# Kernel optimization log

Measured on AMD Instinct MI355X. Metric: run time of the kernel, lower is better.

Reference implementation:

```python
import jax, jax.numpy as jnp
import numpy as np

B, T, C = 8, 2048, 1024
NEG_BIG = -1e30  # exp(NEG_BIG - row_max) underflows to exactly 0 in fp32


def setup_inputs() -> dict:
    key = jax.random.key(0)
    k1, k2 = jax.random.split(key)
    x = jax.random.normal(k1, (B, T, C), dtype=jnp.float32)
    # nn.Linear weight, shape [out, in]; forward computes x @ W^T
    W_H = jax.random.normal(k2, (C, C), dtype=jnp.float32) * (1.0 / np.sqrt(C))
    return {"x": x, "W_H": W_H}


def reference(x, W_H):
    Tdim = x.shape[1]
    xH = jnp.einsum('btc,dc->btd', x, W_H)          # H(x) = x @ W^T, [B,T,C]
    scores = jnp.einsum('btc,bsc->bts', x, xH)       # bilinear scores, [B,T,T]
    # tril_plus_one=True -> strictly-lower-triangular mask (diagonal=-1)
    mask = jnp.tril(jnp.ones((Tdim, Tdim), dtype=bool), k=-1)
    scores = jnp.where(mask, scores, NEG_BIG)
    wei = jax.nn.softmax(scores, axis=-1)            # fully-masked rows -> uniform, zeroed below
    all_masked = ~mask.any(axis=-1)                  # [T], True for row 0
    wei = jnp.where(all_masked[None, :, None], 0.0, wei)
    out = jnp.einsum('bts,bsc->btc', wei, xH)
    return -out
```

## Files before the change

### kernel.cpp

```cpp
#include <hip/hip_runtime.h>
#include <stdint.h>

#define Bn 8
#define Tn 2048
#define Cn 1024
#define Mn (Bn * Tn)
#define NTRI 136
#define NLIN2 72

typedef __attribute__((ext_vector_type(4))) float f32x4;
typedef _Float16 f16;
typedef __attribute__((ext_vector_type(8))) _Float16 f16x8;
typedef uint16_t u16;
typedef uint32_t u32;

static __device__ __forceinline__ u16 f2h(float f) {
  union { f16 h; u16 u; } c; c.h = (f16)f; return c.u;
}
static __device__ __forceinline__ f32x4 mfmaH(f16x8 a, f16x8 b, f32x4 c) {
  return __builtin_amdgcn_mfma_f32_16x16x32_f16(a, b, c, 0, 0, 0);
}
static __device__ __forceinline__ void gld16(const void* g, void* l) {
  __builtin_amdgcn_global_load_lds(
      (const __attribute__((address_space(1))) u32*)g,
      (__attribute__((address_space(3))) u32*)l, 16, 0, 0);
}

__global__ __launch_bounds__(256) void ksplitW(const float* __restrict__ s,
                                               u16* __restrict__ hi) {
  size_t i = ((size_t)blockIdx.x * 256 + threadIdx.x) * 8;
  float4 a = *(const float4*)(s + i), b = *(const float4*)(s + i + 4);
  float f[8] = {a.x, a.y, a.z, a.w, b.x, b.y, b.z, b.w};
  union { u16 u[8]; uint4 v; } H;
#pragma unroll
  for (int j = 0; j < 8; ++j) H.u[j] = f2h(f[j]);
  *(uint4*)(hi + i) = H.v;
}

__global__ __launch_bounds__(256) void ksplitX(const float* __restrict__ s,
                                               u16* __restrict__ hi,
                                               u16* __restrict__ lo) {
  size_t i = ((size_t)blockIdx.x * 256 + threadIdx.x) * 8;
  float4 a = *(const float4*)(s + i), b = *(const float4*)(s + i + 4);
  float f[8] = {a.x, a.y, a.z, a.w, b.x, b.y, b.z, b.w};
  union { u16 u[8]; uint4 v; } H, L;
#pragma unroll
  for (int j = 0; j < 8; ++j) {
    f16 h = (f16)f[j];
    union { f16 h; u16 u; } ch; ch.h = h;
    H.u[j] = ch.u;
    L.u[j] = f2h(f[j] - (float)h);
  }
  *(uint4*)(hi + i) = H.v;
  *(uint4*)(lo + i) = L.v;
}

__global__ __launch_bounds__(256) void k1_xh(const u16* __restrict__ x_h,
                                             const u16* __restrict__ W_h,
                                             u16* __restrict__ xh) {
  __shared__ __align__(16) u16 Ah[8192], Bh[8192];
  const int tid = threadIdx.x;
  const int m0 = blockIdx.x * 128, n0 = blockIdx.y * 128;
  const int wave = tid >> 6, lane = tid & 63;
  const int wrow = (wave >> 1) * 64, wcol = (wave & 1) * 64;
  const int quad = lane >> 4, l16 = lane & 15;

  f32x4 acc[4][4] = {};

  for (int k0 = 0; k0 < Cn; k0 += 64) {
#pragma unroll
    for (int i = 0; i < 4; ++i) {
      int chunk = i * 256 + tid;
      int kk = chunk >> 9, row = (chunk >> 2) & 127, c8 = (chunk & 3) * 8;
      gld16(x_h + (size_t)(m0 + row) * Cn + k0 + kk * 32 + c8, Ah + chunk * 8);
      gld16(W_h + (size_t)(n0 + row) * Cn + k0 + kk * 32 + c8, Bh + chunk * 8);
    }
    __syncthreads();
#pragma unroll
    for (int kk = 0; kk < 2; ++kk) {
      f16x8 a[4], b[4];
#pragma unroll
      for (int i = 0; i < 4; ++i) {
        a[i] = *(const f16x8*)(Ah + kk * 4096 + (wrow + i * 16 + l16) * 32 + quad * 8);
        b[i] = *(const f16x8*)(Bh + kk * 4096 + (wcol + i * 16 + l16) * 32 + quad * 8);
      }
#pragma unroll
      for (int mi = 0; mi < 4; ++mi)
#pragma unroll
        for (int ni = 0; ni < 4; ++ni)
          acc[mi][ni] = mfmaH(a[mi], b[ni], acc[mi][ni]);
    }
    __syncthreads();
  }
#pragma unroll
  for (int mi = 0; mi < 4; ++mi)
#pragma unroll
    for (int ni = 0; ni < 4; ++ni)
#pragma unroll
      for (int r = 0; r < 4; ++r) {
        int row = wrow + mi * 16 + quad * 4 + r;
        int col = wcol + ni * 16 + l16;
        xh[(size_t)(m0 + row) * Cn + n0 + col] = f2h(acc[mi][ni][r]);
      }
}

__global__ __launch_bounds__(512) void k2_scores(const u16* __restrict__ x_h,
                                                 const u16* __restrict__ x_l,
                                                 const u16* __restrict__ xh,
                                                 u16* __restrict__ P,
                                                 float* __restrict__ mt,
                                                 float* __restrict__ lt) {
  __shared__ __align__(16) union {
    struct { u16 Ah[3][4096], Al[3][4096], Bh[3][8192]; } s;
    struct { float Mrow[4][128]; float Lrow[4][128]; } e;
  } u;
  const int tid = threadIdx.x;
  const int bL = blockIdx.y;
  const int lin = blockIdx.x;
  int qt = 0, cum = 0;
  while (cum + ((qt >> 1) + 1) <= lin) { cum += (qt >> 1) + 1; qt++; }
  const int bcol = lin - cum;
  const int t0 = qt * 128, s0 = bcol * 256;
  const int wave = tid >> 6, lane = tid & 63;
  const int wc = wave & 3;
  const int wrow = (wave >> 2) * 64, wcol = wc * 64;
  const int quad = lane >> 4, l16 = lane & 15;

  f32x4 acc[4][4] = {};
  const size_t abase = ((size_t)bL * Tn + t0) * Cn;
  const size_t bbase = ((size_t)bL * Tn + s0) * Cn;
  const int arow = tid >> 2, ac8 = (tid & 3) * 8;

  auto stage = [&](int buf, int k0) {
    size_t aoff = abase + (size_t)arow * Cn + k0 + ac8;
    gld16(x_h + aoff, &u.s.Ah[buf][tid * 8]);
    gld16(x_l + aoff, &u.s.Al[buf][tid * 8]);
#pragma unroll
    for (int i = 0; i < 2; ++i) {
      int ch = i * 512 + tid;
      int row = ch >> 2, c8 = (ch & 3) * 8;
      gld16(xh + bbase + (size_t)row * Cn + k0 + c8, &u.s.Bh[buf][ch * 8]);
    }
  };

  stage(0, 0);
  stage(1, 32);
  int cur = 0;
#pragma unroll 1
  for (int kidx = 0; kidx < 32; ++kidx) {
    if (kidx < 31) {
      asm volatile("s_waitcnt vmcnt(4) lgkmcnt(0)" ::: "memory");
    } else {
      asm volatile("s_waitcnt vmcnt(0) lgkmcnt(0)" ::: "memory");
    }
    __builtin_amdgcn_s_barrier();
    __builtin_amdgcn_sched_barrier(0);
    if (kidx < 30) {
      int tgt = cur >= 1 ? cur - 1 : 2;
      stage(tgt, (kidx + 2) * 32);
    }
    f16x8 b[4];
#pragma unroll
    for (int ni = 0; ni < 4; ++ni)
      b[ni] = *(const f16x8*)&u.s.Bh[cur][(wcol + ni * 16 + l16) * 32 + quad * 8];
#pragma unroll
    for (int mi = 0; mi < 4; ++mi) {
      f16x8 ah = *(const f16x8*)&u.s.Ah[cur][(wrow + mi * 16 + l16) * 32 + quad * 8];
      f16x8 al = *(const f16x8*)&u.s.Al[cur][(wrow + mi * 16 + l16) * 32 + quad * 8];
#pragma unroll
      for (int ni = 0; ni < 4; ++ni) {
        acc[mi][ni] = mfmaH(ah, b[ni], acc[mi][ni]);
        acc[mi][ni] = mfmaH(al, b[ni], acc[mi][ni]);
      }
    }
    cur = cur < 2 ? cur + 1 : 0;
  }

  float rm[4][4];
#pragma unroll
  for (int mi = 0; mi < 4; ++mi)
#pragma unroll
    for (int r = 0; r < 4; ++r) {
      int row = wrow + mi * 16 + quad * 4 + r;
      float m = -1e30f;
#pragma unroll
      for (int ni = 0; ni < 4; ++ni) {
        int scol = s0 + wcol + ni * 16 + l16;
        if (scol >= t0 + row) acc[mi][ni][r] = -1e30f;
        m = fmaxf(m, acc[mi][ni][r]);
      }
      m = fmaxf(m, __shfl_xor(m, 1));
      m = fmaxf(m, __shfl_xor(m, 2));
      m = fmaxf(m, __shfl_xor(m, 4));
      m = fmaxf(m, __shfl_xor(m, 8));
      rm[mi][r] = m;
    }
  if (l16 == 0) {
#pragma unroll
    for (int mi = 0; mi < 4; ++mi)
#pragma unroll
      for (int r = 0; r < 4; ++r)
        u.e.Mrow[wc][wrow + mi * 16 + quad * 4 + r] = rm[mi][r];
  }
  __syncthreads();
  const int h2 = (wc >> 1) * 2;
  float rs[4][4];
#pragma unroll
  for (int mi = 0; mi < 4; ++mi)
#pragma unroll
    for (int r = 0; r < 4; ++r) {
      int row = wrow + mi * 16 + quad * 4 + r;
      float m2 = fmaxf(u.e.Mrow[h2][row], u.e.Mrow[h2 + 1][row]);
      float s = 0.f;
#pragma unroll
      for (int ni = 0; ni < 4; ++ni) {
        int scol = s0 + wcol + ni * 16 + l16;
        float p = (scol < t0 + row) ? __expf(acc[mi][ni][r] - m2) : 0.0f;
        acc[mi][ni][r] = p;
        s += p;
      }
      s += __shfl_xor(s, 1);
      s += __shfl_xor(s, 2);
      s += __shfl_xor(s, 4);
      s += __shfl_xor(s, 8);
      rs[mi][r] = s;
      rm[mi][r] = m2;
    }
  if (l16 == 0) {
#pragma unroll
    for (int mi = 0; mi < 4; ++mi)
#pragma unroll
      for (int r = 0; r < 4; ++r)
        u.e.Lrow[wc][wrow + mi * 16 + quad * 4 + r] = rs[mi][r];
  }
  __syncthreads();
  const int st128 = bcol * 2 + (wc >> 1);
  if (st128 <= qt) {
    if ((wc & 1) == 0 && l16 == 0) {
#pragma unroll
      for (int mi = 0; mi < 4; ++mi)
#pragma unroll
        for (int r = 0; r < 4; ++r) {
          int row = wrow + mi * 16 + quad * 4 + r;
          size_t rI = (size_t)bL * Tn + t0 + row;
          mt[rI * 16 + st128] = rm[mi][r];
          lt[rI * 16 + st128] = u.e.Lrow[wc][row] + u.e.Lrow[wc + 1][row];
        }
    }
    const size_t pbase = (size_t)(bL * NTRI + qt * (qt + 1) / 2 + st128) * 16384;
#pragma unroll
    for (int mi = 0; mi < 4; ++mi)
#pragma unroll
      for (int ni = 0; ni < 4; ++ni)
#pragma unroll
        for (int r = 0; r < 4; ++r) {
          int row = wrow + mi * 16 + quad * 4 + r;
          int pcol = (wcol & 64) + ni * 16 + l16;
          P[pbase + row * 128 + pcol] = f2h(acc[mi][ni][r]);
        }
  }
}

__global__ __launch_bounds__(256) void k3_stats(const float* __restrict__ mt,
                                                const float* __restrict__ lt,
                                                float* __restrict__ Mr,
                                                float* __restrict__ Li) {
  int r = blockIdx.x * 256 + threadIdx.x;
  int t = r & (Tn - 1);
  int nt = (t == 0) ? 0 : (((t - 1) >> 7) + 1);
  float M = -1e30f;
  for (int i = 0; i < nt; ++i) M = fmaxf(M, mt[(size_t)r * 16 + i]);
  float L = 0.f;
  for (int i = 0; i < nt; ++i) L += lt[(size_t)r * 16 + i] * __expf(mt[(size_t)r * 16 + i] - M);
  Mr[r] = M;
  Li[r] = (L > 0.f) ? 1.f / L : 0.f;
}

__global__ __launch_bounds__(256) void ktr(const u16* __restrict__ src,
                                           u16* __restrict__ dst) {
  __shared__ __align__(16) u16 S[128 * 136];
  const int t0 = blockIdx.x * 128, c0 = blockIdx.y * 128, b = blockIdx.z;
  const int tid = threadIdx.x;
#pragma unroll
  for (int i = 0; i < 8; ++i) {
    int chunk = tid + i * 256;
    int row = chunk >> 4, c8 = (chunk & 15) * 8;
    uint4 v = *(const uint4*)(src + ((size_t)b * Tn + t0 + row) * Cn + c0 + c8);
    *(uint4*)(S + row * 136 + c8) = v;
  }
  __syncthreads();
#pragma unroll
  for (int i = 0; i < 8; ++i) {
    int chunk = tid + i * 256;
    int crow = chunk >> 4, t8 = (chunk & 15) * 8;
    union { u16 s[8]; uint4 v; } o;
#pragma unroll
    for (int j = 0; j < 8; ++j) o.s[j] = S[(t8 + j) * 136 + crow];
    *(uint4*)(dst + ((size_t)b * Cn + c0 + crow) * Tn + t0 + t8) = o.v;
  }
}

__global__ __launch_bounds__(256) void k4_out(const u16* __restrict__ P,
                                              const u16* __restrict__ xhT,
                                              const float* __restrict__ mt,
                                              const float* __restrict__ Mr,
                                              const float* __restrict__ Li,
                                              float* __restrict__ out) {
  __shared__ __align__(16) u16 Ap[8192], Bp[8192];
  const int tid = threadIdx.x;
  const int tt = 15 - blockIdx.x;
  const int cn = blockIdx.y, bL = blockIdx.z;
  const int t0 = tt * 128, c0 = cn * 128;
  const int wave = tid >> 6, lane = tid & 63;
  const int wrow = (wave >> 1) * 64, wcol = (wave & 1) * 64;
  const int quad = lane >> 4, l16 = lane & 15;

  f32x4 acc[4][4] = {};
  size_t rI[4]; float MrL[4], LiL[4];
#pragma unroll
  for (int mi = 0; mi < 4; ++mi) {
    rI[mi] = (size_t)bL * Tn + t0 + wrow + mi * 16 + l16;
    MrL[mi] = Mr[rI[mi]];
    LiL[mi] = Li[rI[mi]];
  }
  const size_t bbase = ((size_t)bL * Cn + c0) * Tn;

  for (int st = 0; st <= tt; ++st) {
    f16 ah[4];
#pragma unroll
    for (int mi = 0; mi < 4; ++mi)
      ah[mi] = (f16)(__expf(mt[rI[mi] * 16 + st] - MrL[mi]) * LiL[mi]);
    const size_t pbase = (size_t)(bL * NTRI + tt * (tt + 1) / 2 + st) * 16384;
#pragma unroll 1
    for (int kl = 0; kl < 128; kl += 64) {
#pragma unroll
      for (int i = 0; i < 4; ++i) {
        int chunk = i * 256 + tid;
        int kk = chunk >> 9, row = (chunk >> 2) & 127, c8 = (chunk & 3) * 8;
        gld16(P + pbase + (size_t)row * 128 + kl + kk * 32 + c8, Ap + chunk * 8);
        gld16(xhT + bbase + (size_t)row * Tn + st * 128 + kl + kk * 32 + c8, Bp + chunk * 8);
      }
      __syncthreads();
#pragma unroll
      for (int kk = 0; kk < 2; ++kk) {
        f16x8 a[4], b[4];
#pragma unroll
        for (int i = 0; i < 4; ++i) {
          a[i] = *(const f16x8*)(Ap + kk * 4096 + (wrow + i * 16 + l16) * 32 + quad * 8);
          f16x8 sv;
#pragma unroll
          for (int j = 0; j < 8; ++j) sv[j] = ah[i];
          a[i] = a[i] * sv;
          b[i] = *(const f16x8*)(Bp + kk * 4096 + (wcol + i * 16 + l16) * 32 + quad * 8);
        }
#pragma unroll
        for (int mi = 0; mi < 4; ++mi)
#pragma unroll
          for (int ni = 0; ni < 4; ++ni)
            acc[mi][ni] = mfmaH(a[mi], b[ni], acc[mi][ni]);
      }
      __syncthreads();
    }
  }
#pragma unroll
  for (int mi = 0; mi < 4; ++mi)
#pragma unroll
    for (int ni = 0; ni < 4; ++ni)
#pragma unroll
      for (int r = 0; r < 4; ++r) {
        int row = wrow + mi * 16 + quad * 4 + r;
        int col = wcol + ni * 16 + l16;
        out[((size_t)bL * Tn + t0 + row) * Cn + c0 + col] = -acc[mi][ni][r];
      }
}

extern "C" void kernel_launch(void* const* d_in, const int* in_sizes, int n_in,
                              void* d_out, int out_size, void* d_ws, size_t ws_size,
                              hipStream_t stream) {
  (void)in_sizes; (void)n_in; (void)out_size;
  const float* x = (const float*)d_in[0];
  const float* W = (const float*)d_in[1];
  float* out = (float*)d_out;

  const size_t FULL_NEED = 3ull * Mn * Cn * 2 + (size_t)Bn * NTRI * 16384 * 2 +
                           (size_t)Cn * Cn * 2 + 2ull * Mn * 16 * 4 + 2ull * Mn * 4;
  const int nch = (ws_size >= FULL_NEED) ? 1 : 2;
  const int nb = Bn / nch;
  const size_t rowsC = (size_t)nb * Tn;
  const size_t sA = rowsC * Cn * 2;

  char* p = (char*)d_ws;
  u16* x_h = (u16*)p; p += sA;
  u16* xLT = (u16*)p; p += sA;
  u16* xh  = (u16*)p; p += sA;
  u16* Pp  = (u16*)p; p += (size_t)nb * NTRI * 16384 * 2;
  u16* W_h = (u16*)p; p += (size_t)Cn * Cn * 2;
  float* mt = (float*)p; p += rowsC * 16 * 4;
  float* lt = (float*)p; p += rowsC * 16 * 4;
  float* Mr = (float*)p; p += rowsC * 4;
  float* Li = (float*)p; p += rowsC * 4;

  dim3 blk(256);
  ksplitW<<<dim3(Cn * Cn / 2048), blk, 0, stream>>>(W, W_h);
  for (int c = 0; c < nch; ++c) {
    const float* xc = x + (size_t)c * rowsC * Cn;
    float* oc = out + (size_t)c * rowsC * Cn;
    ksplitX<<<dim3((u32)(rowsC * Cn / 2048)), blk, 0, stream>>>(xc, x_h, xLT);
    k1_xh<<<dim3((u32)(rowsC / 128), Cn / 128), blk, 0, stream>>>(x_h, W_h, xh);
    k2_scores<<<dim3(NLIN2, nb), dim3(512), 0, stream>>>(x_h, xLT, xh, Pp, mt, lt);
    k3_stats<<<dim3((u32)(rowsC / 256)), blk, 0, stream>>>(mt, lt, Mr, Li);
    ktr<<<dim3(Tn / 128, Cn / 128, nb), blk, 0, stream>>>(xh, xLT);
    k4_out<<<dim3(16, Cn / 128, nb), blk, 0, stream>>>(Pp, xLT, mt, Mr, Li, oc);
  }
}
```

Baseline: 413.3 us.

## Widen k4_out tile to 128x256 with triple-buffered LDS pipeline and precomputed alphas

The output GEMM kernel now uses 512 threads and 128x256 output tiles, halving the number of column blocks so each P tile is reused across more columns. The K loop is restructured into 32-wide steps with a three-stage LDS ring buffer, issuing loads two steps ahead with explicit vmcnt waits and one barrier per step instead of two. The per-row softmax scaling factors are precomputed once into LDS instead of recomputing exp per row and tile in registers. Risks are lower occupancy from larger blocks and LDS use, and fewer blocks for load balance across the triangular workload.

```diff
diff --git a/kernel.cpp b/kernel.cpp
--- a/kernel.cpp
+++ b/kernel.cpp
@@ -300,68 +300,94 @@
   }
 }
 
-__global__ __launch_bounds__(256) void k4_out(const u16* __restrict__ P,
+__global__ __launch_bounds__(512) void k4_out(const u16* __restrict__ P,
                                               const u16* __restrict__ xhT,
                                               const float* __restrict__ mt,
                                               const float* __restrict__ Mr,
                                               const float* __restrict__ Li,
                                               float* __restrict__ out) {
-  __shared__ __align__(16) u16 Ap[8192], Bp[8192];
+  __shared__ __align__(16) u16 Ap[3][4096], Bp[3][8192];
+  __shared__ u16 alphaLds[16 * 128];
   const int tid = threadIdx.x;
   const int tt = 15 - blockIdx.x;
   const int cn = blockIdx.y, bL = blockIdx.z;
-  const int t0 = tt * 128, c0 = cn * 128;
+  const int t0 = tt * 128, c0 = cn * 256;
   const int wave = tid >> 6, lane = tid & 63;
-  const int wrow = (wave >> 1) * 64, wcol = (wave & 1) * 64;
+  const int wc = wave & 3;
+  const int wrow = (wave >> 2) * 64, wcol = wc * 64;
   const int quad = lane >> 4, l16 = lane & 15;
 
+  {
+    const size_t rbase = (size_t)bL * Tn + t0;
+#pragma unroll
+    for (int j = 0; j < 4; ++j) {
+      int idx = tid + j * 512;
+      int stp = idx >> 7, row = idx & 127;
+      float a = 0.f;
+      if (stp <= tt)
+        a = __expf(mt[(rbase + row) * 16 + stp] - Mr[rbase + row]) * Li[rbase + row];
+      alphaLds[idx] = f2h(a);
+    }
+  }
+
   f32x4 acc[4][4] = {};
-  size_t rI[4]; float MrL[4], LiL[4];
-#pragma unroll
-  for (int mi = 0; mi < 4; ++mi) {
-    rI[mi] = (size_t)bL * Tn + t0 + wrow + mi * 16 + l16;
-    MrL[mi] = Mr[rI[mi]];
-    LiL[mi] = Li[rI[mi]];
-  }
   const size_t bbase = ((size_t)bL * Cn + c0) * Tn;
-
-  for (int st = 0; st <= tt; ++st) {
-    f16 ah[4];
-#pragma unroll
-    for (int mi = 0; mi < 4; ++mi)
-      ah[mi] = (f16)(__expf(mt[rI[mi] * 16 + st] - MrL[mi]) * LiL[mi]);
-    const size_t pbase = (size_t)(bL * NTRI + tt * (tt + 1) / 2 + st) * 16384;
+  const size_t ptile0 = (size_t)(bL * NTRI + tt * (tt + 1) / 2) * 16384;
+
+  auto stage = [&](int buf, int step) {
+    const int st = step >> 2, k32 = (step & 3) * 32;
+    {
+      int row = tid >> 2, c8 = (tid & 3) * 8;
+      gld16(P + ptile0 + (size_t)st * 16384 + row * 128 + k32 + c8,
+            &Ap[buf][tid * 8]);
+    }
+#pragma unroll
+    for (int i = 0; i < 2; ++i) {
+      int ch = i * 512 + tid;
+      int row = ch >> 2, c8 = (ch & 3) * 8;
+      gld16(xhT + bbase + (size_t)row * Tn + st * 128 + k32 + c8,
+            &Bp[buf][ch * 8]);
+    }
+  };
+
+  const int steps = 4 * (tt + 1);
+  stage(0, 0);
+  stage(1, 1);
+  int cur = 0;
 #pragma unroll 1
-    for (int kl = 0; kl < 128; kl += 64) {
-#pragma unroll
-      for (int i = 0; i < 4; ++i) {
-        int chunk = i * 256 + tid;
-        int kk = chunk >> 9, row = (chunk >> 2) & 127, c8 = (chunk & 3) * 8;
-        gld16(P + pbase + (size_t)row * 128 + kl + kk * 32 + c8, Ap + chunk * 8);
-        gld16(xhT + bbase + (size_t)row * Tn + st * 128 + kl + kk * 32 + c8, Bp + chunk * 8);
-      }
-      __syncthreads();
-#pragma unroll
-      for (int kk = 0; kk < 2; ++kk) {
-        f16x8 a[4], b[4];
-#pragma unroll
-        for (int i = 0; i < 4; ++i) {
-          a[i] = *(const f16x8*)(Ap + kk * 4096 + (wrow + i * 16 + l16) * 32 + quad * 8);
-          f16x8 sv;
-#pragma unroll
-          for (int j = 0; j < 8; ++j) sv[j] = ah[i];
-          a[i] = a[i] * sv;
-          b[i] = *(const f16x8*)(Bp + kk * 4096 + (wcol + i * 16 + l16) * 32 + quad * 8);
-        }
-#pragma unroll
-        for (int mi = 0; mi < 4; ++mi)
-#pragma unroll
-          for (int ni = 0; ni < 4; ++ni)
-            acc[mi][ni] = mfmaH(a[mi], b[ni], acc[mi][ni]);
-      }
-      __syncthreads();
-    }
-  }
+  for (int s = 0; s < steps; ++s) {
+    if (s < steps - 1) {
+      asm volatile("s_waitcnt vmcnt(3) lgkmcnt(0)" ::: "memory");
+    } else {
+      asm volatile("s_waitcnt vmcnt(0) lgkmcnt(0)" ::: "memory");
+    }
+    __builtin_amdgcn_s_barrier();
+    __builtin_amdgcn_sched_barrier(0);
+    if (s < steps - 2) {
+      int tgt = cur >= 1 ? cur - 1 : 2;
+      stage(tgt, s + 2);
+    }
+    const int st = s >> 2;
+    f16x8 b[4];
+#pragma unroll
+    for (int ni = 0; ni < 4; ++ni)
+      b[ni] = *(const f16x8*)&Bp[cur][(wcol + ni * 16 + l16) * 32 + quad * 8];
+#pragma unroll
+    for (int mi = 0; mi < 4; ++mi) {
+      union { u16 u; f16 h; } ca;
+      ca.u = alphaLds[st * 128 + wrow + mi * 16 + l16];
+      f16x8 sv;
+#pragma unroll
+      for (int j = 0; j < 8; ++j) sv[j] = ca.h;
+      f16x8 a = *(const f16x8*)&Ap[cur][(wrow + mi * 16 + l16) * 32 + quad * 8];
+      a = a * sv;
+#pragma unroll
+      for (int ni = 0; ni < 4; ++ni)
+        acc[mi][ni] = mfmaH(a, b[ni], acc[mi][ni]);
+    }
+    cur = cur < 2 ? cur + 1 : 0;
+  }
+
 #pragma unroll
   for (int mi = 0; mi < 4; ++mi)
 #pragma unroll
@@ -410,6 +436,6 @@
     k2_scores<<<dim3(NLIN2, nb), dim3(512), 0, stream>>>(x_h, xLT, xh, Pp, mt, lt);
     k3_stats<<<dim3((u32)(rowsC / 256)), blk, 0, stream>>>(mt, lt, Mr, Li);
     ktr<<<dim3(Tn / 128, Cn / 128, nb), blk, 0, stream>>>(xh, xLT);
-    k4_out<<<dim3(16, Cn / 128, nb), blk, 0, stream>>>(Pp, xLT, mt, Mr, Li, oc);
-  }
-}
+    k4_out<<<dim3(16, Cn / 256, nb), dim3(512), 0, stream>>>(Pp, xLT, mt, Mr, Li, oc);
+  }
+}
```

After: 384.6 us. 7.0% less time.
